# Optimization experiments

Measured on AMD Instinct MI355X. Metric: run time of the kernel, lower is better.

Reference implementation:

```python
import jax, jax.numpy as jnp
import numpy as np
from jax import lax

B, T, D, H, O = 32, 512, 512, 1024, 512


def setup_inputs() -> dict:
    key = jax.random.key(0)
    ks = jax.random.split(key, 7)
    s = lambda fan_in: 1.0 / np.sqrt(fan_in)
    return {
        "x": jax.random.normal(ks[0], (B, T, D), jnp.float32),
        "Wx0": jax.random.normal(ks[1], (D, 4 * H), jnp.float32) * s(D),
        "Wh0": jax.random.normal(ks[2], (H, 4 * H), jnp.float32) * s(H),
        "b0": jnp.zeros((4 * H,), jnp.float32),
        "Wx1": jax.random.normal(ks[3], (H, 4 * H), jnp.float32) * s(H),
        "Wh1": jax.random.normal(ks[4], (H, 4 * H), jnp.float32) * s(H),
        "b1": jnp.zeros((4 * H,), jnp.float32),
        "Wd": jax.random.normal(ks[5], (H, O), jnp.float32) * s(H),
        "bd": jnp.zeros((O,), jnp.float32),
    }


def _lstm_cell(c, h, inp, Wx, Wh, b):
    # flax OptimizedLSTMCell: fused gate GEMM, gate order i, f, g, o
    z = inp @ Wx + h @ Wh + b  # [B, 4H]
    i, f, g, o = jnp.split(z, 4, axis=-1)
    c_new = jax.nn.sigmoid(f) * c + jax.nn.sigmoid(i) * jnp.tanh(g)
    h_new = jax.nn.sigmoid(o) * jnp.tanh(c_new)
    return c_new, h_new


def reference(x, Wx0, Wh0, b0, Wx1, Wh1, b1, Wd, bd):
    b = x.shape[0]
    h = Wh0.shape[0]
    zero = jnp.zeros((b, h), x.dtype)
    carry0 = ((zero, zero), (zero, zero))  # ((c0, h0), (c1, h1)), zeros like flax default

    def step(carry, xt):
        (c0, h0), (c1, h1) = carry
        c0, h0 = _lstm_cell(c0, h0, xt, Wx0, Wh0, b0)
        c1, h1 = _lstm_cell(c1, h1, h0, Wx1, Wh1, b1)
        return ((c0, h0), (c1, h1)), h1

    xs = jnp.swapaxes(x, 0, 1)  # [T, B, D] for scan over time
    _, ys = lax.scan(step, carry0, xs)
    y = jnp.swapaxes(ys, 0, 1)  # [B, T, H]
    return y @ Wd + bd  # [B, T, O]
```

## Files before the change

kernel.cpp:

```cpp
#include <hip/hip_runtime.h>


typedef _Float16 half8  __attribute__((ext_vector_type(8)));
typedef float    floatx4 __attribute__((ext_vector_type(4)));

#define WREC_OFF   0UL
#define WX0_OFF    25165824UL
#define WD_OFF     29360128UL
#define XH_OFF     30408704UL
#define ZX0_OFF    47185920UL
#define H1_OFF     181403648UL
#define H0_OFF     214958080UL
#define FLAGS_OFF  248512512UL

__device__ __forceinline__ float fsig(float x){ return 1.0f/(1.0f + __expf(-x)); }
__device__ __forceinline__ float ftanhf(float x){
  float e = __expf(2.0f*fabsf(x));
  float r = 1.0f - 2.0f/(e + 1.0f);
  return copysignf(r, x);
}

__global__ void conv_wrec(const float* __restrict__ Wh0,
                          const float* __restrict__ Wx1,
                          const float* __restrict__ Wh1,
                          _Float16* __restrict__ out){
  int idx = blockIdx.x*256 + threadIdx.x;
  if (idx >= 256*3*128*16) return;
  int c  = idx & 15;
  int t1 = idx >> 4;
  int kc = t1 & 127;
  int t2 = t1 >> 7;
  int mat = t2 % 3;
  int wg  = t2 / 3;
  const float* W = (mat==0) ? Wh0 : (mat==1) ? Wx1 : Wh1;
  int col = (c>>2)*1024 + wg*4 + (c&3);
  _Float16* o = out + (size_t)idx*8;
  #pragma unroll
  for (int j=0;j<8;++j) o[j] = (_Float16)W[(kc*8+j)*4096 + col];
}

__global__ void conv_wx0(const float* __restrict__ W, _Float16* __restrict__ out){
  int idx = blockIdx.x*256 + threadIdx.x;
  if (idx >= 256*64*16) return;
  int c  = idx & 15;
  int kc = (idx >> 4) & 63;
  int wg = idx >> 10;
  int col = (c>>2)*1024 + wg*4 + (c&3);
  _Float16* o = out + (size_t)idx*8;
  #pragma unroll
  for (int j=0;j<8;++j) o[j] = (_Float16)W[(kc*8+j)*4096 + col];
}

__global__ void conv_wd(const float* __restrict__ W, _Float16* __restrict__ out){
  int idx = blockIdx.x*256 + threadIdx.x;
  if (idx >= 32*128*16) return;
  int c  = idx & 15;
  int kc = (idx >> 4) & 127;
  int nt = idx >> 11;
  int col = nt*16 + c;
  _Float16* o = out + (size_t)idx*8;
  #pragma unroll
  for (int j=0;j<8;++j) o[j] = (_Float16)W[(kc*8+j)*512 + col];
}

__global__ void conv_x(const float* __restrict__ x, _Float16* __restrict__ xh){
  int idx = blockIdx.x*256 + threadIdx.x;
  if (idx >= 2097152) return;
  int dq = idx & 127;
  int bt = idx >> 7;
  int b  = bt & 31;
  int t  = bt >> 5;
  float4 v = ((const float4*)x)[(size_t)(b*512 + t)*128 + dq];
  _Float16* o = xh + (size_t)idx*4;
  o[0]=(_Float16)v.x; o[1]=(_Float16)v.y; o[2]=(_Float16)v.z; o[3]=(_Float16)v.w;
}

__global__ __launch_bounds__(64) void zx0_gemm(const _Float16* __restrict__ xh,
                                               const _Float16* __restrict__ wx0a,
                                               const float* __restrict__ b0,
                                               _Float16* __restrict__ zx0){
  int t   = blockIdx.x;
  int wgg = blockIdx.y;
  int l = threadIdx.x, q = l>>4, c = l&15;
  floatx4 acc[2][4];
  #pragma unroll
  for (int g=0; g<4; ++g){
    int wg = wgg*4+g;
    float bv = b0[(c>>2)*1024 + wg*4 + (c&3)];
    acc[0][g] = (floatx4){bv,bv,bv,bv};
    acc[1][g] = (floatx4){bv,bv,bv,bv};
  }
  #pragma unroll 4
  for (int ks=0; ks<16; ++ks){
    int kc = ks*4 + q;
    half8 a0 = *(const half8*)(xh + (t*32      + c)*512 + kc*8);
    half8 a1 = *(const half8*)(xh + (t*32 + 16 + c)*512 + kc*8);
    #pragma unroll
    for (int g=0; g<4; ++g){
      int wg = wgg*4+g;
      half8 b = *(const half8*)(wx0a + ((size_t)(wg*64 + kc)*16 + c)*8);
      acc[0][g] = __builtin_amdgcn_mfma_f32_16x16x32_f16(a0,b,acc[0][g],0,0,0);
      acc[1][g] = __builtin_amdgcn_mfma_f32_16x16x32_f16(a1,b,acc[1][g],0,0,0);
    }
  }
  #pragma unroll
  for (int g=0; g<4; ++g){
    int wg = wgg*4+g;
    #pragma unroll
    for (int mt=0; mt<2; ++mt)
      #pragma unroll
      for (int r=0;r<4;++r){
        int m = mt*16 + q*4 + r;
        zx0[((size_t)(t*256 + wg)*32 + m)*16 + c] = (_Float16)acc[mt][g][r];
      }
  }
}

#define AF(base, ks)  (*(const half8*)((base) + (ks)*32))
#define BF(w, ks)     (*(const half8*)((w) + (((ks)*4 + q)*16 + c)*8))

__device__ __forceinline__ void gates_store(floatx4 acc, float* cs,
    _Float16* dst, int g, int c, int mt, int q, int wg){
  #pragma unroll
  for (int r=0;r<4;++r){
    float v0 = acc[r];
    float v1 = __shfl_xor(v0, 4, 64);
    float v2 = __shfl_xor(v0, 8, 64);
    float v3 = __shfl_xor(v1, 8, 64);
    float zi = (g==0)?v0:(g==1)?v1:(g==2)?v2:v3;
    float zf = (g==0)?v1:(g==1)?v0:(g==2)?v3:v2;
    float zg = (g==0)?v2:(g==1)?v3:(g==2)?v0:v1;
    float zo = (g==0)?v3:(g==1)?v2:(g==2)?v1:v0;
    float cn = fsig(zf)*cs[r] + fsig(zi)*ftanhf(zg);
    cs[r] = cn;
    float hv = fsig(zo)*ftanhf(cn);
    unsigned hb16 = (unsigned)__builtin_bit_cast(unsigned short, (_Float16)hv);
    unsigned up   = (unsigned)__shfl_xor((int)hb16, 1, 64);
    if (g==0 && (c&1)==0)
      __hip_atomic_store((unsigned*)(dst + (mt*16 + q*4 + r)*1024 + wg*4 + c),
                         hb16 | (up<<16),
                         __ATOMIC_RELAXED, __HIP_MEMORY_SCOPE_AGENT);
  }
}

__global__ __launch_bounds__(128, 1) void lstm_persist(
    const _Float16* __restrict__ wrec, const _Float16* __restrict__ zx0,
    const float* __restrict__ b1g, _Float16* __restrict__ h0a,
    _Float16* __restrict__ h1a, unsigned int* __restrict__ flags)
{
  extern __shared__ _Float16 lds[];
  _Float16* w0  = lds;
  _Float16* w1  = lds + 16384;
  _Float16* w2  = lds + 32768;

  const int wg = blockIdx.x, tid = threadIdx.x;
  const int wv = tid>>6, l = tid&63, q = l>>4, c = l&15;
  const int g = (c>>2);
  const int mt = wv;
  const int row = mt*16 + c;
  const int grp = wg >> 3;

  unsigned int* gcnt = flags + grp*64;

  {
    const uint4* src = (const uint4*)(wrec + (size_t)wg*49152);
    uint4* dst = (uint4*)lds;
    for (int i=tid; i<6144; i+=128) dst[i] = src[i];
  }
  float c0[4] = {0,0,0,0}, c1[4] = {0,0,0,0};
  const float b1v = b1g[g*1024 + wg*4 + (c&3)];
  __syncthreads();

  {
    const _Float16* zsrc = zx0 + ((size_t)wg*32 + mt*16 + q*4)*16 + c;
    floatx4 a;
    a[0]=(float)zsrc[0]; a[1]=(float)zsrc[16]; a[2]=(float)zsrc[32]; a[3]=(float)zsrc[48];
    gates_store(a, c0, h0a, g, c, mt, q, wg);
  }

  for (int t=0; t<512; ++t){
    __syncthreads();

    const unsigned tgt = (unsigned)(t+1);
    if (tid == 0)
      __hip_atomic_fetch_add(gcnt, 1u, __ATOMIC_RELAXED,
                             __HIP_MEMORY_SCOPE_AGENT);

    int tn = (t<511) ? t+1 : 511;
    const _Float16* zsrc = zx0 + ((size_t)(tn*256 + wg)*32 + mt*16 + q*4)*16 + c;
    float pz0=(float)zsrc[0], pz1=(float)zsrc[16], pz2=(float)zsrc[32], pz3=(float)zsrc[48];

    if (wv == 0){
      const unsigned thr = 8u*tgt;
      const unsigned int* myleaf = flags + l*64;
      for (;;){
        unsigned v = 0xffffffffu;
        if (l < 32)
          v = __hip_atomic_load(myleaf, __ATOMIC_RELAXED,
                                __HIP_MEMORY_SCOPE_AGENT);
        if (__ballot(v >= thr) == 0xffffffffffffffffULL) break;
        __builtin_amdgcn_s_sleep(1);
      }
    }
    __syncthreads();

    const _Float16* h0c = h0a + (size_t)t*32768 + row*1024 + q*8;
    const _Float16* h1p = h1a + (size_t)(t-1)*32768 + row*1024 + q*8;
    half8 H1[32], H0[32];
    if (t > 0){
      #pragma unroll
      for (int s=0; s<32; ++s) H1[s] = AF(h1p, s);
    }
    #pragma unroll
    for (int s=0; s<32; ++s) H0[s] = AF(h0c, s);

    floatx4 aA0={0,0,0,0}, aA1={0,0,0,0};
    floatx4 aB0={b1v,b1v,b1v,b1v}, aB1={0,0,0,0};
    floatx4 aC0={0,0,0,0}, aC1={0,0,0,0};
    if (t > 0){
      #pragma unroll
      for (int s=0; s<16; ++s){
        aC0 = __builtin_amdgcn_mfma_f32_16x16x32_f16(H1[s],    BF(w2,s),    aC0,0,0,0);
        aC1 = __builtin_amdgcn_mfma_f32_16x16x32_f16(H1[16+s], BF(w2,16+s), aC1,0,0,0);
      }
    }
    #pragma unroll
    for (int s=0; s<16; ++s){
      aB0 = __builtin_amdgcn_mfma_f32_16x16x32_f16(H0[s],    BF(w1,s),    aB0,0,0,0);
      aB1 = __builtin_amdgcn_mfma_f32_16x16x32_f16(H0[16+s], BF(w1,16+s), aB1,0,0,0);
      aA0 = __builtin_amdgcn_mfma_f32_16x16x32_f16(H0[s],    BF(w0,s),    aA0,0,0,0);
      aA1 = __builtin_amdgcn_mfma_f32_16x16x32_f16(H0[16+s], BF(w0,16+s), aA1,0,0,0);
    }
    {
      floatx4 z1 = (aB0+aB1)+(aC0+aC1);
      gates_store(z1, c1, h1a + (size_t)t*32768, g, c, mt, q, wg);
    }
    if (t < 511){
      floatx4 z0 = aA0+aA1;
      z0[0]+=pz0; z0[1]+=pz1; z0[2]+=pz2; z0[3]+=pz3;
      gates_store(z0, c0, h0a + (size_t)(t+1)*32768, g, c, mt, q, wg);
    }
  }
}

__global__ __launch_bounds__(256) void wd_gemm(const _Float16* __restrict__ h1a,
                                               const _Float16* __restrict__ wda,
                                               const float* __restrict__ bd,
                                               float* __restrict__ y){
  int mb = blockIdx.x;
  int nb = blockIdx.y;
  int tid = threadIdx.x, wv = tid>>6, l = tid&63, q = l>>4, c = l&15;
  int mt = wv & 1, nh = wv >> 1;
  floatx4 acc[4];
  #pragma unroll
  for (int gg=0; gg<4; ++gg) acc[gg] = (floatx4){0.f,0.f,0.f,0.f};
  const _Float16* arow = h1a + (size_t)(mb*32 + mt*16 + c)*1024;
  #pragma unroll 4
  for (int ks=0; ks<32; ++ks){
    int kc = ks*4 + q;
    half8 a = *(const half8*)(arow + kc*8);
    #pragma unroll
    for (int gg=0; gg<4; ++gg){
      int nt = nb*8 + nh*4 + gg;
      half8 b = *(const half8*)(wda + ((size_t)(nt*128 + kc)*16 + c)*8);
      acc[gg] = __builtin_amdgcn_mfma_f32_16x16x32_f16(a,b,acc[gg],0,0,0);
    }
  }
  #pragma unroll
  for (int gg=0; gg<4; ++gg){
    int o = nb*128 + nh*64 + gg*16 + c;
    float bdv = bd[o];
    #pragma unroll
    for (int r=0;r<4;++r){
      int row = mb*32 + mt*16 + q*4 + r;
      int tt = row >> 5, bb = row & 31;
      y[(size_t)bb*262144 + tt*512 + o] = acc[gg][r] + bdv;
    }
  }
}

extern "C" void kernel_launch(void* const* d_in, const int* in_sizes, int n_in,
                              void* d_out, int out_size, void* d_ws, size_t ws_size,
                              hipStream_t stream){
  const float* x   = (const float*)d_in[0];
  const float* Wx0 = (const float*)d_in[1];
  const float* Wh0 = (const float*)d_in[2];
  const float* b0  = (const float*)d_in[3];
  const float* Wx1 = (const float*)d_in[4];
  const float* Wh1 = (const float*)d_in[5];
  const float* b1  = (const float*)d_in[6];
  const float* Wd  = (const float*)d_in[7];
  const float* bd  = (const float*)d_in[8];
  float* y = (float*)d_out;
  char* ws = (char*)d_ws;

  _Float16* wrec = (_Float16*)(ws + WREC_OFF);
  _Float16* wx0a = (_Float16*)(ws + WX0_OFF);
  _Float16* wda  = (_Float16*)(ws + WD_OFF);
  _Float16* xh   = (_Float16*)(ws + XH_OFF);
  _Float16* zx0  = (_Float16*)(ws + ZX0_OFF);
  _Float16* h1a  = (_Float16*)(ws + H1_OFF);
  _Float16* h0a  = (_Float16*)(ws + H0_OFF);
  unsigned int* flags = (unsigned int*)(ws + FLAGS_OFF);

  hipMemsetAsync(flags, 0, 24576, stream);
  conv_wrec<<<dim3(6144), dim3(256), 0, stream>>>(Wh0, Wx1, Wh1, wrec);
  conv_wx0 <<<dim3(1024), dim3(256), 0, stream>>>(Wx0, wx0a);
  conv_wd  <<<dim3(256),  dim3(256), 0, stream>>>(Wd, wda);
  conv_x   <<<dim3(8192), dim3(256), 0, stream>>>(x, xh);
  zx0_gemm <<<dim3(512,64), dim3(64), 0, stream>>>(xh, wx0a, b0, zx0);
  hipFuncSetAttribute((const void*)lstm_persist,
                      hipFuncAttributeMaxDynamicSharedMemorySize, 98304);
  lstm_persist<<<dim3(256), dim3(128), 98304, stream>>>(wrec, zx0, b1, h0a, h1a, flags);
  wd_gemm  <<<dim3(512,4), dim3(256), 0, stream>>>(h1a, wda, bd, y);
}
```

Before: 5.307 ms.

## Split persistent LSTM into layer-0 and layer-1 block groups with pipelined barriers

The persistent kernel is restructured so 64 blocks run only layer 0 (four hidden slices each) and 128 blocks run only layer 1 (two slices each), instead of every block doing both layers for one slice. Each group synchronises through its own flag/go signalling scheme, with layer 1 trailing layer 0 by a step, so the two layers can run as a pipeline and the per-step grid barrier no longer serialises both layers. This raises LDS use to 128KB per block and adds cross-group flag traffic and busy-wait spinning without sleep, which risks contention and imbalance between the groups.

```diff
diff --git a/kernel.cpp b/kernel.cpp
--- a/kernel.cpp
+++ b/kernel.cpp
@@ -120,7 +120,7 @@
 #define BF(w, ks)     (*(const half8*)((w) + (((ks)*4 + q)*16 + c)*8))
 
 __device__ __forceinline__ void gates_store(floatx4 acc, float* cs,
-    _Float16* dst, int g, int c, int mt, int q, int wg){
+    _Float16* dst, int g, int c, int mt, int q, int wgo){
   #pragma unroll
   for (int r=0;r<4;++r){
     float v0 = acc[r];
@@ -137,11 +137,14 @@
     unsigned hb16 = (unsigned)__builtin_bit_cast(unsigned short, (_Float16)hv);
     unsigned up   = (unsigned)__shfl_xor((int)hb16, 1, 64);
     if (g==0 && (c&1)==0)
-      __hip_atomic_store((unsigned*)(dst + (mt*16 + q*4 + r)*1024 + wg*4 + c),
+      __hip_atomic_store((unsigned*)(dst + (mt*16 + q*4 + r)*1024 + wgo*4 + c),
                          hb16 | (up<<16),
                          __ATOMIC_RELAXED, __HIP_MEMORY_SCOPE_AGENT);
   }
 }
+
+#define LDU(p) __hip_atomic_load((p), __ATOMIC_RELAXED, __HIP_MEMORY_SCOPE_AGENT)
+#define STU(p,v) __hip_atomic_store((p), (v), __ATOMIC_RELAXED, __HIP_MEMORY_SCOPE_AGENT)
 
 __global__ __launch_bounds__(128, 1) void lstm_persist(
     const _Float16* __restrict__ wrec, const _Float16* __restrict__ zx0,
@@ -149,96 +152,176 @@
     _Float16* __restrict__ h1a, unsigned int* __restrict__ flags)
 {
   extern __shared__ _Float16 lds[];
-  _Float16* w0  = lds;
-  _Float16* w1  = lds + 16384;
-  _Float16* w2  = lds + 32768;
 
   const int wg = blockIdx.x, tid = threadIdx.x;
   const int wv = tid>>6, l = tid&63, q = l>>4, c = l&15;
   const int g = (c>>2);
   const int mt = wv;
   const int row = mt*16 + c;
-  const int grp = wg >> 3;
-
-  unsigned int* gcnt = flags + grp*64;
-
-  {
-    const uint4* src = (const uint4*)(wrec + (size_t)wg*49152);
-    uint4* dst = (uint4*)lds;
-    for (int i=tid; i<6144; i+=128) dst[i] = src[i];
-  }
-  float c0[4] = {0,0,0,0}, c1[4] = {0,0,0,0};
-  const float b1v = b1g[g*1024 + wg*4 + (c&3)];
-  __syncthreads();
-
-  {
-    const _Float16* zsrc = zx0 + ((size_t)wg*32 + mt*16 + q*4)*16 + c;
-    floatx4 a;
-    a[0]=(float)zsrc[0]; a[1]=(float)zsrc[16]; a[2]=(float)zsrc[32]; a[3]=(float)zsrc[48];
-    gates_store(a, c0, h0a, g, c, mt, q, wg);
-  }
-
-  for (int t=0; t<512; ++t){
+
+  unsigned int* slotA = flags;
+  unsigned int* goA   = flags + 4096;
+  unsigned int* slotB = flags + 16384;
+  unsigned int* goB   = flags + 24576;
+
+  if (wg < 64){
+    const int a = wg;
+    #pragma unroll
+    for (int j=0;j<4;++j){
+      const uint4* src = (const uint4*)(wrec + ((size_t)(4*a+j)*3 + 0)*16384);
+      uint4* dst = (uint4*)(lds + j*16384);
+      for (int i=tid;i<2048;i+=128) dst[i]=src[i];
+    }
+    float c0s[4][4] = {{0,0,0,0},{0,0,0,0},{0,0,0,0},{0,0,0,0}};
+
+    #pragma unroll
+    for (int j=0;j<4;++j){
+      const _Float16* zsrc = zx0 + ((size_t)(4*a+j)*32 + mt*16 + q*4)*16 + c;
+      floatx4 z;
+      z[0]=(float)zsrc[0]; z[1]=(float)zsrc[16]; z[2]=(float)zsrc[32]; z[3]=(float)zsrc[48];
+      gates_store(z, c0s[j], h0a, g, c, mt, q, 4*a+j);
+    }
     __syncthreads();
-
-    const unsigned tgt = (unsigned)(t+1);
-    if (tid == 0)
-      __hip_atomic_fetch_add(gcnt, 1u, __ATOMIC_RELAXED,
-                             __HIP_MEMORY_SCOPE_AGENT);
-
-    int tn = (t<511) ? t+1 : 511;
-    const _Float16* zsrc = zx0 + ((size_t)(tn*256 + wg)*32 + mt*16 + q*4)*16 + c;
-    float pz0=(float)zsrc[0], pz1=(float)zsrc[16], pz2=(float)zsrc[32], pz3=(float)zsrc[48];
-
-    if (wv == 0){
-      const unsigned thr = 8u*tgt;
-      const unsigned int* myleaf = flags + l*64;
-      for (;;){
-        unsigned v = 0xffffffffu;
-        if (l < 32)
-          v = __hip_atomic_load(myleaf, __ATOMIC_RELAXED,
-                                __HIP_MEMORY_SCOPE_AGENT);
-        if (__ballot(v >= thr) == 0xffffffffffffffffULL) break;
-        __builtin_amdgcn_s_sleep(1);
-      }
-    }
-    __syncthreads();
-
-    const _Float16* h0c = h0a + (size_t)t*32768 + row*1024 + q*8;
-    const _Float16* h1p = h1a + (size_t)(t-1)*32768 + row*1024 + q*8;
-    half8 H1[32], H0[32];
-    if (t > 0){
-      #pragma unroll
-      for (int s=0; s<32; ++s) H1[s] = AF(h1p, s);
-    }
-    #pragma unroll
-    for (int s=0; s<32; ++s) H0[s] = AF(h0c, s);
-
-    floatx4 aA0={0,0,0,0}, aA1={0,0,0,0};
-    floatx4 aB0={b1v,b1v,b1v,b1v}, aB1={0,0,0,0};
-    floatx4 aC0={0,0,0,0}, aC1={0,0,0,0};
-    if (t > 0){
-      #pragma unroll
-      for (int s=0; s<16; ++s){
-        aC0 = __builtin_amdgcn_mfma_f32_16x16x32_f16(H1[s],    BF(w2,s),    aC0,0,0,0);
-        aC1 = __builtin_amdgcn_mfma_f32_16x16x32_f16(H1[16+s], BF(w2,16+s), aC1,0,0,0);
-      }
-    }
-    #pragma unroll
-    for (int s=0; s<16; ++s){
-      aB0 = __builtin_amdgcn_mfma_f32_16x16x32_f16(H0[s],    BF(w1,s),    aB0,0,0,0);
-      aB1 = __builtin_amdgcn_mfma_f32_16x16x32_f16(H0[16+s], BF(w1,16+s), aB1,0,0,0);
-      aA0 = __builtin_amdgcn_mfma_f32_16x16x32_f16(H0[s],    BF(w0,s),    aA0,0,0,0);
-      aA1 = __builtin_amdgcn_mfma_f32_16x16x32_f16(H0[16+s], BF(w0,16+s), aA1,0,0,0);
-    }
-    {
-      floatx4 z1 = (aB0+aB1)+(aC0+aC1);
-      gates_store(z1, c1, h1a + (size_t)t*32768, g, c, mt, q, wg);
-    }
-    if (t < 511){
-      floatx4 z0 = aA0+aA1;
-      z0[0]+=pz0; z0[1]+=pz1; z0[2]+=pz2; z0[3]+=pz3;
-      gates_store(z0, c0, h0a + (size_t)(t+1)*32768, g, c, mt, q, wg);
+    if (tid==0) STU(slotA + a*64, 1u);
+
+    for (int k=0;k<511;++k){
+      const unsigned tgt = (unsigned)(k+1);
+      float pz[4][4];
+      #pragma unroll
+      for (int j=0;j<4;++j){
+        const _Float16* zsrc = zx0 + ((size_t)((k+1)*256 + 4*a+j)*32 + mt*16 + q*4)*16 + c;
+        pz[j][0]=(float)zsrc[0]; pz[j][1]=(float)zsrc[16];
+        pz[j][2]=(float)zsrc[32]; pz[j][3]=(float)zsrc[48];
+      }
+      if (a==0 && wv==0){
+        for(;;){
+          unsigned v = LDU(slotA + l*64);
+          if (__ballot(v >= tgt) == 0xffffffffffffffffULL) break;
+        }
+        #pragma unroll
+        for (int m=0;m<3;++m) STU(goA + (size_t)(m*64+l)*64, tgt);
+      } else if (a!=0 && tid==0){
+        while (LDU(goA + (size_t)a*64) < tgt) ;
+      }
+      __syncthreads();
+
+      const _Float16* h0c = h0a + (size_t)k*32768 + row*1024 + q*8;
+      half8 H0[32];
+      #pragma unroll
+      for (int s=0;s<32;++s) H0[s] = AF(h0c, s);
+
+      floatx4 acc[4], acc2[4];
+      #pragma unroll
+      for (int j=0;j<4;++j){ acc[j]=(floatx4){0,0,0,0}; acc2[j]=(floatx4){0,0,0,0}; }
+      #pragma unroll
+      for (int s=0;s<16;++s){
+        #pragma unroll
+        for (int j=0;j<4;++j){
+          acc[j]  = __builtin_amdgcn_mfma_f32_16x16x32_f16(H0[s],    BF(lds + j*16384, s),    acc[j], 0,0,0);
+          acc2[j] = __builtin_amdgcn_mfma_f32_16x16x32_f16(H0[16+s], BF(lds + j*16384, 16+s), acc2[j],0,0,0);
+        }
+      }
+      #pragma unroll
+      for (int j=0;j<4;++j){
+        floatx4 z = acc[j] + acc2[j];
+        z[0]+=pz[j][0]; z[1]+=pz[j][1]; z[2]+=pz[j][2]; z[3]+=pz[j][3];
+        gates_store(z, c0s[j], h0a + (size_t)(k+1)*32768, g, c, mt, q, 4*a+j);
+      }
+      __syncthreads();
+      if (tid==0) STU(slotA + a*64, (unsigned)(k+2));
+    }
+    if (a==0 && wv==0){
+      for(;;){
+        unsigned v = LDU(slotA + l*64);
+        if (__ballot(v >= 512u) == 0xffffffffffffffffULL) break;
+      }
+      #pragma unroll
+      for (int m=0;m<3;++m) STU(goA + (size_t)(m*64+l)*64, 512u);
+    }
+  } else {
+    const int b = wg - 64;
+    #pragma unroll
+    for (int j=0;j<2;++j){
+      const uint4* src = (const uint4*)(wrec + ((size_t)(2*b+j)*3 + 1)*16384);
+      uint4* dst = (uint4*)(lds + j*16384);
+      for (int i=tid;i<2048;i+=128) dst[i]=src[i];
+    }
+    #pragma unroll
+    for (int j=0;j<2;++j){
+      const uint4* src = (const uint4*)(wrec + ((size_t)(2*b+j)*3 + 2)*16384);
+      uint4* dst = (uint4*)(lds + (2+j)*16384);
+      for (int i=tid;i<2048;i+=128) dst[i]=src[i];
+    }
+    float c1s[2][4] = {{0,0,0,0},{0,0,0,0}};
+    float b1v[2];
+    #pragma unroll
+    for (int j=0;j<2;++j) b1v[j] = b1g[g*1024 + (2*b+j)*4 + (c&3)];
+
+    for (int k=0;k<512;++k){
+      const unsigned tgtA = (unsigned)(k+1);
+      if (b==0 && wv==0){
+        if (k > 0){
+          for(;;){
+            unsigned va = LDU(slotB + l*64);
+            unsigned vb = LDU(slotB + (size_t)(64+l)*64);
+            if (__ballot((va >= (unsigned)k) & (vb >= (unsigned)k)) ==
+                0xffffffffffffffffULL) break;
+          }
+          #pragma unroll
+          for (int m=0;m<2;++m) STU(goB + (size_t)(m*64+l)*64, (unsigned)k);
+        }
+        if (l==0){
+          while (LDU(goA + (size_t)64*64) < tgtA) ;
+        }
+      } else if (b!=0 && tid==0){
+        while (LDU(goA + (size_t)(64+b)*64) < tgtA) ;
+        if (k > 0)
+          while (LDU(goB + (size_t)b*64) < (unsigned)k) ;
+      }
+      __syncthreads();
+
+      const _Float16* h0c = h0a + (size_t)k*32768 + row*1024 + q*8;
+      half8 H0[32];
+      #pragma unroll
+      for (int s=0;s<32;++s) H0[s] = AF(h0c, s);
+      half8 H1[32];
+      if (k > 0){
+        const _Float16* h1p = h1a + (size_t)(k-1)*32768 + row*1024 + q*8;
+        #pragma unroll
+        for (int s=0;s<32;++s) H1[s] = AF(h1p, s);
+      }
+
+      floatx4 acc[2], acc2[2];
+      #pragma unroll
+      for (int j=0;j<2;++j){
+        acc[j] = (floatx4){b1v[j],b1v[j],b1v[j],b1v[j]};
+        acc2[j] = (floatx4){0,0,0,0};
+      }
+      #pragma unroll
+      for (int s=0;s<16;++s){
+        #pragma unroll
+        for (int j=0;j<2;++j){
+          acc[j]  = __builtin_amdgcn_mfma_f32_16x16x32_f16(H0[s],    BF(lds + j*16384, s),    acc[j], 0,0,0);
+          acc2[j] = __builtin_amdgcn_mfma_f32_16x16x32_f16(H0[16+s], BF(lds + j*16384, 16+s), acc2[j],0,0,0);
+        }
+      }
+      if (k > 0){
+        #pragma unroll
+        for (int s=0;s<16;++s){
+          #pragma unroll
+          for (int j=0;j<2;++j){
+            acc[j]  = __builtin_amdgcn_mfma_f32_16x16x32_f16(H1[s],    BF(lds + (2+j)*16384, s),    acc[j], 0,0,0);
+            acc2[j] = __builtin_amdgcn_mfma_f32_16x16x32_f16(H1[16+s], BF(lds + (2+j)*16384, 16+s), acc2[j],0,0,0);
+          }
+        }
+      }
+      #pragma unroll
+      for (int j=0;j<2;++j){
+        floatx4 z = acc[j] + acc2[j];
+        gates_store(z, c1s[j], h1a + (size_t)k*32768, g, c, mt, q, 2*b+j);
+      }
+      __syncthreads();
+      if (tid==0) STU(slotB + (size_t)b*64, (unsigned)(k+1));
     }
   }
 }
@@ -303,14 +386,14 @@
   _Float16* h0a  = (_Float16*)(ws + H0_OFF);
   unsigned int* flags = (unsigned int*)(ws + FLAGS_OFF);
 
-  hipMemsetAsync(flags, 0, 24576, stream);
+  hipMemsetAsync(flags, 0, 131072, stream);
   conv_wrec<<<dim3(6144), dim3(256), 0, stream>>>(Wh0, Wx1, Wh1, wrec);
   conv_wx0 <<<dim3(1024), dim3(256), 0, stream>>>(Wx0, wx0a);
   conv_wd  <<<dim3(256),  dim3(256), 0, stream>>>(Wd, wda);
   conv_x   <<<dim3(8192), dim3(256), 0, stream>>>(x, xh);
   zx0_gemm <<<dim3(512,64), dim3(64), 0, stream>>>(xh, wx0a, b0, zx0);
   hipFuncSetAttribute((const void*)lstm_persist,
-                      hipFuncAttributeMaxDynamicSharedMemorySize, 98304);
-  lstm_persist<<<dim3(256), dim3(128), 98304, stream>>>(wrec, zx0, b1, h0a, h1a, flags);
+                      hipFuncAttributeMaxDynamicSharedMemorySize, 131072);
+  lstm_persist<<<dim3(192), dim3(128), 131072, stream>>>(wrec, zx0, b1, h0a, h1a, flags);
   wd_gemm  <<<dim3(512,4), dim3(256), 0, stream>>>(h1a, wda, bd, y);
 }
```

Measured after the change: 5.323 ms. No clear change (+0.3%).

## Replace grouped atomic-counter barrier with per-wave slots and central go flags

Applied to the files above, without the earlier changes.

The per-timestep grid barrier in the persistent LSTM kernel is rebuilt. Each wave now publishes its progress by storing the step number into its own slot after draining its outstanding memory ops. A single master wave in workgroup 0 polls all slots with 64-bit loads and then writes a per-workgroup go flag. Every other wave spins on its own go flag, which removes the block-wide __syncthreads and the atomic fetch-adds from each step. The cost is an extra hop through the master and relaxed-only ordering for the h visibility that the barrier protects.

```diff
diff --git a/kernel.cpp b/kernel.cpp
--- a/kernel.cpp
+++ b/kernel.cpp
@@ -118,6 +118,11 @@
 
 #define AF(base, ks)  (*(const half8*)((base) + (ks)*32))
 #define BF(w, ks)     (*(const half8*)((w) + (((ks)*4 + q)*16 + c)*8))
+
+#define LDU(p)  __hip_atomic_load((p),  __ATOMIC_RELAXED, __HIP_MEMORY_SCOPE_AGENT)
+#define STU(p,v) __hip_atomic_store((p), (v), __ATOMIC_RELAXED, __HIP_MEMORY_SCOPE_AGENT)
+#define LDU64(p) __hip_atomic_load((const unsigned long long*)(p), \
+                                   __ATOMIC_RELAXED, __HIP_MEMORY_SCOPE_AGENT)
 
 __device__ __forceinline__ void gates_store(floatx4 acc, float* cs,
     _Float16* dst, int g, int c, int mt, int q, int wg){
@@ -158,9 +163,9 @@
   const int g = (c>>2);
   const int mt = wv;
   const int row = mt*16 + c;
-  const int grp = wg >> 3;
-
-  unsigned int* gcnt = flags + grp*64;
+
+  unsigned int* slot = flags + (size_t)wg*64;
+  unsigned int* go   = flags + 16384 + (size_t)wg*64;
 
   {
     const uint4* src = (const uint4*)(wrec + (size_t)wg*49152);
@@ -177,32 +182,35 @@
     a[0]=(float)zsrc[0]; a[1]=(float)zsrc[16]; a[2]=(float)zsrc[32]; a[3]=(float)zsrc[48];
     gates_store(a, c0, h0a, g, c, mt, q, wg);
   }
+  asm volatile("s_waitcnt vmcnt(0)" ::: "memory");
+  if (l == 0) STU(slot + wv, 1u);
 
   for (int t=0; t<512; ++t){
-    __syncthreads();
-
     const unsigned tgt = (unsigned)(t+1);
-    if (tid == 0)
-      __hip_atomic_fetch_add(gcnt, 1u, __ATOMIC_RELAXED,
-                             __HIP_MEMORY_SCOPE_AGENT);
 
     int tn = (t<511) ? t+1 : 511;
     const _Float16* zsrc = zx0 + ((size_t)(tn*256 + wg)*32 + mt*16 + q*4)*16 + c;
     float pz0=(float)zsrc[0], pz1=(float)zsrc[16], pz2=(float)zsrc[32], pz3=(float)zsrc[48];
 
-    if (wv == 0){
-      const unsigned thr = 8u*tgt;
-      const unsigned int* myleaf = flags + l*64;
+    if (wg == 0 && wv == 0){
       for (;;){
-        unsigned v = 0xffffffffu;
-        if (l < 32)
-          v = __hip_atomic_load(myleaf, __ATOMIC_RELAXED,
-                                __HIP_MEMORY_SCOPE_AGENT);
-        if (__ballot(v >= thr) == 0xffffffffffffffffULL) break;
-        __builtin_amdgcn_s_sleep(1);
+        int ok = 1;
+        #pragma unroll
+        for (int m=0; m<4; ++m){
+          unsigned long long v = LDU64(flags + (size_t)(l*4+m)*64);
+          ok &= (int)(((unsigned)v >= tgt) & ((unsigned)(v>>32) >= tgt));
+        }
+        if (__ballot(ok) == 0xffffffffffffffffULL) break;
       }
-    }
-    __syncthreads();
+      #pragma unroll
+      for (int m=0; m<4; ++m)
+        STU(flags + 16384 + (size_t)(l*4+m)*64, tgt);
+    } else {
+      if (l == 0){
+        while (LDU(go) < tgt) ;
+      }
+    }
+    asm volatile("" ::: "memory");
 
     const _Float16* h0c = h0a + (size_t)t*32768 + row*1024 + q*8;
     const _Float16* h1p = h1a + (size_t)(t-1)*32768 + row*1024 + q*8;
@@ -240,6 +248,8 @@
       z0[0]+=pz0; z0[1]+=pz1; z0[2]+=pz2; z0[3]+=pz3;
       gates_store(z0, c0, h0a + (size_t)(t+1)*32768, g, c, mt, q, wg);
     }
+    asm volatile("s_waitcnt vmcnt(0)" ::: "memory");
+    if (l == 0) STU(slot + wv, (unsigned)(t+2));
   }
 }
 
@@ -303,7 +313,7 @@
   _Float16* h0a  = (_Float16*)(ws + H0_OFF);
   unsigned int* flags = (unsigned int*)(ws + FLAGS_OFF);
 
-  hipMemsetAsync(flags, 0, 24576, stream);
+  hipMemsetAsync(flags, 0, 131072, stream);
   conv_wrec<<<dim3(6144), dim3(256), 0, stream>>>(Wh0, Wx1, Wh1, wrec);
   conv_wx0 <<<dim3(1024), dim3(256), 0, stream>>>(Wx0, wx0a);
   conv_wd  <<<dim3(256),  dim3(256), 0, stream>>>(Wd, wda);
```

Result: no change. 5.227 ms (-1.5%).
